# Performance work log

Hardware: AMD Instinct MI355X
Metric: run time of the kernel (lower is better)

Reference implementation:

```python
import jax, jax.numpy as jnp
import numpy as np

SIZE = 128
DELTA = 1.0
NUM_SHELLS = SIZE // 2  # 64 shells up to Nyquist; corners beyond Nyquist are discarded
DROP_DC = False
ALPHA = None
EPS = 1e-8


def _make_shell_idx(n, delta):
    # integer-frequency radial coordinate, same grid as torch.fft.fftfreq(n)*n
    f = np.fft.fftfreq(n) * n
    fx, fy, fz = np.meshgrid(f, f, f, indexing="ij")
    r = np.sqrt(fx * fx + fy * fy + fz * fz)
    idx = np.floor(r / delta).astype(np.int32)
    # voxels past the Nyquist shell go to a discard bucket (index NUM_SHELLS)
    idx = np.where(idx < NUM_SHELLS, idx, NUM_SHELLS)
    return idx


def setup_inputs() -> dict:
    key = jax.random.key(0)
    k1, k2 = jax.random.split(key)
    shape = (8, 1, SIZE, SIZE, SIZE)
    img_ref = jax.random.normal(k1, shape, dtype=jnp.float32)
    img_pred = jax.random.normal(k2, shape, dtype=jnp.float32)
    shell_idx = jnp.asarray(_make_shell_idx(SIZE, DELTA))
    return {"img_ref": img_ref, "img_pred": img_pred, "shell_idx": shell_idx}


def reference(img_ref, img_pred, shell_idx):
    B = img_ref.shape[0] * img_ref.shape[1]
    V = SIZE * SIZE * SIZE
    F1 = jnp.fft.fftn(img_ref, axes=(-3, -2, -1)).reshape(B, V)
    F2 = jnp.fft.fftn(img_pred, axes=(-3, -2, -1)).reshape(B, V)
    idx = shell_idx.reshape(V)

    # per-shell reductions (single pass, replaces num_shells dense mask-multiplies)
    cross = (F1 * jnp.conj(F2)).real          # Re sum F1 conj(F2) per shell
    p1 = (F1.real ** 2 + F1.imag ** 2)
    p2 = (F2.real ** 2 + F2.imag ** 2)

    seg = jax.vmap(lambda x: jax.ops.segment_sum(x, idx, num_segments=NUM_SHELLS + 1))
    num = seg(cross)[:, :NUM_SHELLS]          # [B, num_shells], drop discard bucket
    d1 = seg(p1)[:, :NUM_SHELLS]
    d2 = seg(p2)[:, :NUM_SHELLS]

    fsc = num / (jnp.sqrt(d1 * d2) + EPS)     # [B, num_shells]

    if ALPHA is not None:
        freq = (jnp.arange(NUM_SHELLS, dtype=jnp.float32) + 0.5) * DELTA / SIZE
        fsc = fsc * (freq ** ALPHA)
    if DROP_DC:
        fsc = fsc[:, 1:]

    loss = 1.0 - jnp.mean(fsc ** 2)
    return loss
```

## Files before the change

### kernel.cpp

```cpp
#include <hip/hip_runtime.h>
#include <math.h>

#define N      128
#define LOGN   7
#define NSQ    (N * N)
#define VOL    (N * N * N)
#define NSHELL 64
#define BTOT   8
#define FPI    3.14159265358979323846f

#define TL     16
#define TP     (TL + 1)

__device__ inline float2* fft16(float2* A, float2* B, int t) {
    const int j5 = t & 31;
    const int lg = (t >> 5) << 1;
    float2* src = A;
    float2* dst = B;
#pragma unroll
    for (int s = 0; s < 6; s += 2) {
        const int Ns = 1 << s;
        const int m  = j5 & (Ns - 1);
        const int cc = j5 >> s;
        const int e0 = (cc << (s + 2)) + m;
        float s2, c2;
        __sincosf(-FPI * (float)m / (float)(2 * Ns), &s2, &c2);
        const float cw = c2 * c2 - s2 * s2;
        const float sw = 2.f * c2 * s2;
        __syncthreads();
#pragma unroll
        for (int l = 0; l < 2; ++l) {
            const int line = lg + l;
            const float2 a  = src[ j5       * TP + line];
            const float2 cv = src[(j5 + 32) * TP + line];
            const float2 b  = src[(j5 + 64) * TP + line];
            const float2 d  = src[(j5 + 96) * TP + line];
            const float wbx = b.x * cw - b.y * sw, wby = b.x * sw + b.y * cw;
            const float wdx = d.x * cw - d.y * sw, wdy = d.x * sw + d.y * cw;
            const float Apx = a.x + wbx, Apy = a.y + wby;
            const float Amx = a.x - wbx, Amy = a.y - wby;
            const float Bpx = cv.x + wdx, Bpy = cv.y + wdy;
            const float Bmx = cv.x - wdx, Bmy = cv.y - wdy;
            const float t0x = Bpx * c2 - Bpy * s2, t0y = Bpx * s2 + Bpy * c2;
            const float t1x = Bmx * c2 - Bmy * s2, t1y = Bmx * s2 + Bmy * c2;
            dst[(e0)          * TP + line] = make_float2(Apx + t0x, Apy + t0y);
            dst[(e0 + Ns)     * TP + line] = make_float2(Amx + t1y, Amy - t1x);
            dst[(e0 + 2 * Ns) * TP + line] = make_float2(Apx - t0x, Apy - t0y);
            dst[(e0 + 3 * Ns) * TP + line] = make_float2(Amx - t1y, Amy + t1x);
        }
        float2* tmp = src; src = dst; dst = tmp;
    }
    {
        const int m   = t & 63;
        const int grp = (t >> 6) << 2;
        float sw, cw;
        __sincosf(-FPI * (float)m / 64.f, &sw, &cw);
        __syncthreads();
#pragma unroll
        for (int l = 0; l < 4; ++l) {
            const int line = grp + l;
            const float2 v0 = src[m * TP + line];
            const float2 v1 = src[(m + 64) * TP + line];
            const float wx = v1.x * cw - v1.y * sw;
            const float wy = v1.x * sw + v1.y * cw;
            dst[m * TP + line]        = make_float2(v0.x + wx, v0.y + wy);
            dst[(m + 64) * TP + line] = make_float2(v0.x - wx, v0.y - wy);
        }
    }
    __syncthreads();
    return dst;
}

__global__ __launch_bounds__(256) void k_fftz_pack(const float* __restrict__ ref,
                                                   const float* __restrict__ pred,
                                                   float2* __restrict__ Z, int b0) {
    __shared__ float2 A[N * TP], B[N * TP];
    const int t  = threadIdx.x;
    const int yt = blockIdx.x & 7;
    const int x  = (blockIdx.x >> 3) & (N - 1);
    const int bl = blockIdx.x >> 10;
    const size_t inbase = (size_t)(b0 + bl) * VOL + (size_t)x * NSQ + (size_t)yt * TL * N;
    const size_t zbase  = (size_t)bl * VOL + (size_t)x * NSQ + (size_t)yt * TL * N;
#pragma unroll
    for (int i = 0; i < 8; ++i) {
        const int elem = i * 256 + t;
        const int z = elem & (N - 1);
        const int j = elem >> LOGN;
        A[z * TP + j] = make_float2(ref[inbase + elem], pred[inbase + elem]);
    }
    float2* res = fft16(A, B, t);
#pragma unroll
    for (int i = 0; i < 8; ++i) {
        const int elem = i * 256 + t;
        const int z = elem & (N - 1);
        const int j = elem >> LOGN;
        Z[zbase + elem] = res[z * TP + j];
    }
}

__global__ __launch_bounds__(256) void k_fft_strided(float2* __restrict__ Z,
                                                     int stride, int midmul) {
    __shared__ float2 A[N * TP], B[N * TP];
    const int t   = threadIdx.x;
    const int zt  = blockIdx.x & 7;
    const int mid = (blockIdx.x >> 3) & (N - 1);
    const int bl  = blockIdx.x >> 10;
    const size_t base = (size_t)bl * VOL + (size_t)mid * midmul + (size_t)zt * TL;
#pragma unroll
    for (int i = 0; i < 8; ++i) {
        const int elem = i * 256 + t;
        const int zz = elem & (TL - 1);
        const int j  = elem >> 4;
        A[j * TP + zz] = Z[base + (size_t)j * stride + zz];
    }
    float2* res = fft16(A, B, t);
#pragma unroll
    for (int i = 0; i < 8; ++i) {
        const int elem = i * 256 + t;
        const int zz = elem & (TL - 1);
        const int j  = elem >> 4;
        Z[base + (size_t)j * stride + zz] = res[j * TP + zz];
    }
}

__device__ inline int isqrt_i(int r2) {
    int s = (int)sqrtf((float)r2);
    s -= (s * s > r2);
    s += ((s + 1) * (s + 1) <= r2);
    return s;
}

__global__ __launch_bounds__(256) void k_reduce(const float2* __restrict__ Z,
                                                float* __restrict__ accum, int b0) {
    const int tid = threadIdx.x;
    const int bl  = blockIdx.x >> 9;
    const int x   = (blockIdx.x >> 2) & (N - 1);
    const int y0  = (blockIdx.x & 3) * 16;
    const int z   = tid & (N - 1);
    const int ys  = (tid >> 7) * 8;

    const int fx = x - ((x >= 64) ? N : 0);
    const int fz = z - ((z >= 64) ? N : 0);

    if (fx * fx + y0 * y0 >= 4096) return;

    __shared__ float sh[4 * 193];
    for (int i = tid; i < 4 * 193; i += 256) sh[i] = 0.f;
    __syncthreads();

    const int mx = (N - x) & (N - 1);
    const int mz = (N - z) & (N - 1);
    const size_t zb = (size_t)bl * VOL;
    const float2* Ap = Z + zb + (size_t)x  * NSQ + z;
    const float2* Bp = Z + zb + (size_t)mx * NSQ + mz;

    float* bins = sh + (tid & 3) * 193;
    const int fxx = fx * fx;
    const int fzz = fz * fz;

    float aC = 0.f, aP1 = 0.f, aP2 = 0.f;
    int cs = -1;
#pragma unroll
    for (int j = 0; j < 8; ++j) {
        const int y  = y0 + ys + j;
        const int s  = isqrt_i(fxx + y * y + fzz);
        if (s != cs) {
            if (cs >= 0 && cs < NSHELL) {
                atomicAdd(&bins[cs * 3 + 0], aC);
                atomicAdd(&bins[cs * 3 + 1], aP1);
                atomicAdd(&bins[cs * 3 + 2], aP2);
            }
            cs = s; aC = 0.f; aP1 = 0.f; aP2 = 0.f;
        }
        if (s < NSHELL) {
            const float w = (y == 0) ? 1.f : 2.f;
            const int my = (N - y) & (N - 1);
            const float2 Av = Ap[(size_t)y  * N];
            const float2 Bv = Bp[(size_t)my * N];
            const float F1x = 0.5f * (Av.x + Bv.x);
            const float F1y = 0.5f * (Av.y - Bv.y);
            const float F2x = 0.5f * (Av.y + Bv.y);
            const float F2y = 0.5f * (Bv.x - Av.x);
            aC  += w * (F1x * F2x + F1y * F2y);
            aP1 += w * (F1x * F1x + F1y * F1y);
            aP2 += w * (F2x * F2x + F2y * F2y);
        }
    }
    if (cs >= 0 && cs < NSHELL) {
        atomicAdd(&bins[cs * 3 + 0], aC);
        atomicAdd(&bins[cs * 3 + 1], aP1);
        atomicAdd(&bins[cs * 3 + 2], aP2);
    }
    __syncthreads();

    float* acc = accum + (size_t)(b0 + bl) * (NSHELL * 3);
    for (int i = tid; i < NSHELL * 3; i += 256) {
        const float v = sh[i] + sh[193 + i] + sh[2 * 193 + i] + sh[3 * 193 + i];
        atomicAdd(&acc[i], v);
    }
}

__global__ __launch_bounds__(512) void k_final(const float* __restrict__ accum,
                                               float* __restrict__ out) {
    __shared__ float red[8];
    const int tid = threadIdx.x;
    const float* a = accum + (size_t)tid * 3;
    const float fsc = a[0] / (sqrtf(a[1] * a[2]) + 1e-8f);
    float v = fsc * fsc;
#pragma unroll
    for (int off = 32; off > 0; off >>= 1) v += __shfl_down(v, off);
    if ((tid & 63) == 0) red[tid >> 6] = v;
    __syncthreads();
    if (tid == 0) {
        float ssum = 0.f;
#pragma unroll
        for (int i = 0; i < 8; ++i) ssum += red[i];
        out[0] = 1.0f - ssum / 512.0f;
    }
}

extern "C" void kernel_launch(void* const* d_in, const int* in_sizes, int n_in,
                              void* d_out, int out_size, void* d_ws, size_t ws_size,
                              hipStream_t stream) {
    const float* ref  = (const float*)d_in[0];
    const float* pred = (const float*)d_in[1];
    float* out = (float*)d_out;

    char*   ws    = (char*)d_ws;
    float*  accum = (float*)ws;
    float2* Zbuf  = (float2*)(ws + 8192);

    const size_t zbytes = (size_t)VOL * sizeof(float2);
    int cap = 1;
    if (ws_size > 8192) {
        size_t c = (ws_size - 8192) / zbytes;
        cap = (c < 1) ? 1 : (c > BTOT ? BTOT : (int)c);
    }

    hipMemsetAsync(accum, 0, BTOT * NSHELL * 3 * sizeof(float), stream);

    for (int b0 = 0; b0 < BTOT; b0 += cap) {
        const int nb = (BTOT - b0 < cap) ? (BTOT - b0) : cap;
        const int nblk = nb * 1024;
        k_fftz_pack<<<nblk, 256, 0, stream>>>(ref, pred, Zbuf, b0);
        k_fft_strided<<<nblk, 256, 0, stream>>>(Zbuf, N, NSQ);
        k_fft_strided<<<nblk, 256, 0, stream>>>(Zbuf, NSQ, N);
        k_reduce<<<nb * 512, 256, 0, stream>>>(Zbuf, accum, b0);
    }
    k_final<<<1, 512, 0, stream>>>(accum, out);
}
```

Baseline: 313.9 us.

## Fuse final x-axis FFT pass with shell reduction kernel

The last strided FFT pass along x is merged into the shell-reduction kernel. Each block loads columns for z and the mirrored -z, runs the 128-point FFT in shared memory, and bins the results directly, so one full write and re-read of the spectrum buffer is dropped. Blocks whose (y,z) slab lies entirely past Nyquist exit early. In exchange the reduce stage now holds large shared-memory FFT buffers and computes twice as many transforms, some of them redundant.

```diff
diff --git a/kernel.cpp b/kernel.cpp
--- a/kernel.cpp
+++ b/kernel.cpp
@@ -98,20 +98,19 @@
     }
 }
 
-__global__ __launch_bounds__(256) void k_fft_strided(float2* __restrict__ Z,
-                                                     int stride, int midmul) {
+__global__ __launch_bounds__(256) void k_ffty(float2* __restrict__ Z) {
     __shared__ float2 A[N * TP], B[N * TP];
     const int t   = threadIdx.x;
     const int zt  = blockIdx.x & 7;
     const int mid = (blockIdx.x >> 3) & (N - 1);
     const int bl  = blockIdx.x >> 10;
-    const size_t base = (size_t)bl * VOL + (size_t)mid * midmul + (size_t)zt * TL;
+    const size_t base = (size_t)bl * VOL + (size_t)mid * NSQ + (size_t)zt * TL;
 #pragma unroll
     for (int i = 0; i < 8; ++i) {
         const int elem = i * 256 + t;
         const int zz = elem & (TL - 1);
         const int j  = elem >> 4;
-        A[j * TP + zz] = Z[base + (size_t)j * stride + zz];
+        A[j * TP + zz] = Z[base + (size_t)j * N + zz];
     }
     float2* res = fft16(A, B, t);
 #pragma unroll
@@ -119,7 +118,7 @@
         const int elem = i * 256 + t;
         const int zz = elem & (TL - 1);
         const int j  = elem >> 4;
-        Z[base + (size_t)j * stride + zz] = res[j * TP + zz];
+        Z[base + (size_t)j * N + zz] = res[j * TP + zz];
     }
 }
 
@@ -130,71 +129,87 @@
     return s;
 }
 
-__global__ __launch_bounds__(256) void k_reduce(const float2* __restrict__ Z,
-                                                float* __restrict__ accum, int b0) {
-    const int tid = threadIdx.x;
-    const int bl  = blockIdx.x >> 9;
-    const int x   = (blockIdx.x >> 2) & (N - 1);
-    const int y0  = (blockIdx.x & 3) * 16;
-    const int z   = tid & (N - 1);
-    const int ys  = (tid >> 7) * 8;
-
-    const int fx = x - ((x >= 64) ? N : 0);
-    const int fz = z - ((z >= 64) ? N : 0);
-
-    if (fx * fx + y0 * y0 >= 4096) return;
-
+__global__ __launch_bounds__(256) void k_fftx_reduce(const float2* __restrict__ Z,
+                                                     float* __restrict__ accum, int b0) {
+    const int t  = threadIdx.x;
+    const int zr = blockIdx.x & 7;
+    const int y  = (blockIdx.x >> 3) & (N - 1);
+    const int bl = blockIdx.x >> 10;
+    const int z0 = zr * 8;
+    const int fy = y - ((y >= 64) ? N : 0);
+
+    if (fy * fy + z0 * z0 >= 4096) return;
+
+    __shared__ float2 A[N * TP], B[N * TP];
     __shared__ float sh[4 * 193];
-    for (int i = tid; i < 4 * 193; i += 256) sh[i] = 0.f;
-    __syncthreads();
-
-    const int mx = (N - x) & (N - 1);
-    const int mz = (N - z) & (N - 1);
-    const size_t zb = (size_t)bl * VOL;
-    const float2* Ap = Z + zb + (size_t)x  * NSQ + z;
-    const float2* Bp = Z + zb + (size_t)mx * NSQ + mz;
-
-    float* bins = sh + (tid & 3) * 193;
-    const int fxx = fx * fx;
-    const int fzz = fz * fz;
+    for (int i = t; i < 4 * 193; i += 256) sh[i] = 0.f;
+
+    const int my = (N - y) & (N - 1);
+    const size_t zb    = (size_t)bl * VOL;
+    const size_t baseA = zb + (size_t)y  * N + z0;
+    const size_t baseB = zb + (size_t)my * N;
+#pragma unroll
+    for (int i = 0; i < 4; ++i) {
+        const int elem = i * 256 + t;
+        const int zz = elem & 7;
+        const int j  = elem >> 3;
+        A[j * TP + zz] = Z[baseA + (size_t)j * NSQ + zz];
+    }
+#pragma unroll
+    for (int i = 0; i < 4; ++i) {
+        const int elem = i * 256 + t;
+        const int zz = elem & 7;
+        const int j  = elem >> 3;
+        const int mz = (N - z0 - zz) & (N - 1);
+        A[j * TP + 8 + zz] = Z[baseB + (size_t)j * NSQ + mz];
+    }
+
+    float2* res = fft16(A, B, t);
+
+    const int l  = t >> 5;
+    const int x0 = (t & 31) * 4;
+    const int z  = z0 + l;
+    const float w = (z == 0) ? 1.f : 2.f;
+    const int ryz = fy * fy + z * z;
+    float* bins = sh + (t & 3) * 193;
 
     float aC = 0.f, aP1 = 0.f, aP2 = 0.f;
     int cs = -1;
 #pragma unroll
-    for (int j = 0; j < 8; ++j) {
-        const int y  = y0 + ys + j;
-        const int s  = isqrt_i(fxx + y * y + fzz);
+    for (int i = 0; i < 4; ++i) {
+        const int x  = x0 + i;
+        const int fx = x - ((x >= 64) ? N : 0);
+        const int s  = isqrt_i(fx * fx + ryz);
         if (s != cs) {
             if (cs >= 0 && cs < NSHELL) {
-                atomicAdd(&bins[cs * 3 + 0], aC);
-                atomicAdd(&bins[cs * 3 + 1], aP1);
-                atomicAdd(&bins[cs * 3 + 2], aP2);
+                atomicAdd(&bins[cs * 3 + 0], w * aC);
+                atomicAdd(&bins[cs * 3 + 1], w * aP1);
+                atomicAdd(&bins[cs * 3 + 2], w * aP2);
             }
             cs = s; aC = 0.f; aP1 = 0.f; aP2 = 0.f;
         }
         if (s < NSHELL) {
-            const float w = (y == 0) ? 1.f : 2.f;
-            const int my = (N - y) & (N - 1);
-            const float2 Av = Ap[(size_t)y  * N];
-            const float2 Bv = Bp[(size_t)my * N];
+            const int mx = (N - x) & (N - 1);
+            const float2 Av = res[x  * TP + l];
+            const float2 Bv = res[mx * TP + 8 + l];
             const float F1x = 0.5f * (Av.x + Bv.x);
             const float F1y = 0.5f * (Av.y - Bv.y);
             const float F2x = 0.5f * (Av.y + Bv.y);
             const float F2y = 0.5f * (Bv.x - Av.x);
-            aC  += w * (F1x * F2x + F1y * F2y);
-            aP1 += w * (F1x * F1x + F1y * F1y);
-            aP2 += w * (F2x * F2x + F2y * F2y);
+            aC  += F1x * F2x + F1y * F2y;
+            aP1 += F1x * F1x + F1y * F1y;
+            aP2 += F2x * F2x + F2y * F2y;
         }
     }
     if (cs >= 0 && cs < NSHELL) {
-        atomicAdd(&bins[cs * 3 + 0], aC);
-        atomicAdd(&bins[cs * 3 + 1], aP1);
-        atomicAdd(&bins[cs * 3 + 2], aP2);
+        atomicAdd(&bins[cs * 3 + 0], w * aC);
+        atomicAdd(&bins[cs * 3 + 1], w * aP1);
+        atomicAdd(&bins[cs * 3 + 2], w * aP2);
     }
     __syncthreads();
 
     float* acc = accum + (size_t)(b0 + bl) * (NSHELL * 3);
-    for (int i = tid; i < NSHELL * 3; i += 256) {
+    for (int i = t; i < NSHELL * 3; i += 256) {
         const float v = sh[i] + sh[193 + i] + sh[2 * 193 + i] + sh[3 * 193 + i];
         atomicAdd(&acc[i], v);
     }
@@ -243,9 +258,8 @@
         const int nb = (BTOT - b0 < cap) ? (BTOT - b0) : cap;
         const int nblk = nb * 1024;
         k_fftz_pack<<<nblk, 256, 0, stream>>>(ref, pred, Zbuf, b0);
-        k_fft_strided<<<nblk, 256, 0, stream>>>(Zbuf, N, NSQ);
-        k_fft_strided<<<nblk, 256, 0, stream>>>(Zbuf, NSQ, N);
-        k_reduce<<<nb * 512, 256, 0, stream>>>(Zbuf, accum, b0);
+        k_ffty<<<nblk, 256, 0, stream>>>(Zbuf);
+        k_fftx_reduce<<<nblk, 256, 0, stream>>>(Zbuf, accum, b0);
     }
     k_final<<<1, 512, 0, stream>>>(accum, out);
 }
```

Measured after the change: 323.9 us. 3.2% more time.
